# Optimization experiments

Measured on AMD Instinct MI355X. Metric: run time of the kernel, lower is better.

Reference implementation:

```python
import jax, jax.numpy as jnp
import numpy as np

N_HEAD = 8  # config.n_head

def _ln(x, g, b):
    # eqx.nn.LayerNorm, eps=1e-5
    m = x.mean(-1, keepdims=True)
    v = ((x - m) ** 2).mean(-1, keepdims=True)
    return (x - m) / jnp.sqrt(v + 1e-5) * g + b

def _lin(x, w, b):
    # eqx.nn.Linear: weight [out, in]
    return x @ w.T + b

def _heads(t):
    B, T, C = t.shape
    return t.reshape(B, T, N_HEAD, C // N_HEAD).transpose(0, 2, 1, 3)  # [B,H,T,d]

def _merge(t):
    B, H, T, d = t.shape
    return t.transpose(0, 2, 1, 3).reshape(B, T, H * d)

def setup_inputs() -> dict:
    key = jax.random.key(0)
    B, T1, T2, C, INNER, NIN = 4, 4096, 4096, 512, 2048, 2
    ks = jax.random.split(key, 16)
    w = lambda k, *s: 0.02 * jax.random.normal(k, s, dtype=jnp.float32)
    return {
        'x': jax.random.normal(ks[0], (B, T1, C), dtype=jnp.float32),
        'ys': jax.random.normal(ks[1], (NIN, B, T2, C), dtype=jnp.float32),
        'ln1_g': jnp.ones((C,)), 'ln1_b': jnp.zeros((C,)),
        'ln2_g': jnp.ones((NIN, C)), 'ln2_b': jnp.zeros((NIN, C)),
        'ln3_g': jnp.ones((C,)), 'ln3_b': jnp.zeros((C,)),
        'ln4_g': jnp.ones((C,)), 'ln4_b': jnp.zeros((C,)),
        'ln5_g': jnp.ones((C,)), 'ln5_b': jnp.zeros((C,)),
        'ca_wq': w(ks[2], C, C), 'ca_bq': jnp.zeros((C,)),
        'ca_wk': w(ks[3], NIN, C, C), 'ca_bk': jnp.zeros((NIN, C)),
        'ca_wv': w(ks[4], NIN, C, C), 'ca_bv': jnp.zeros((NIN, C)),
        'ca_wo': w(ks[5], C, C), 'ca_bo': jnp.zeros((C,)),
        'sa_wq': w(ks[6], C, C), 'sa_bq': jnp.zeros((C,)),
        'sa_wk': w(ks[7], C, C), 'sa_bk': jnp.zeros((C,)),
        'sa_wv': w(ks[8], C, C), 'sa_bv': jnp.zeros((C,)),
        'sa_wo': w(ks[9], C, C), 'sa_bo': jnp.zeros((C,)),
        'ffn1_w1': w(ks[10], INNER, C), 'ffn1_b1': jnp.zeros((INNER,)),
        'ffn1_w2': w(ks[11], C, INNER), 'ffn1_b2': jnp.zeros((C,)),
        'ffn2_w1': w(ks[12], INNER, C), 'ffn2_b1': jnp.zeros((INNER,)),
        'ffn2_w2': w(ks[13], C, INNER), 'ffn2_b2': jnp.zeros((C,)),
    }

def reference(x, ys, ln1_g, ln1_b, ln2_g, ln2_b, ln3_g, ln3_b, ln4_g, ln4_b, ln5_g, ln5_b,
              ca_wq, ca_bq, ca_wk, ca_bk, ca_wv, ca_bv, ca_wo, ca_bo,
              sa_wq, sa_bq, sa_wk, sa_bk, sa_wv, sa_bv, sa_wo, sa_bo,
              ffn1_w1, ffn1_b1, ffn1_w2, ffn1_b2, ffn2_w1, ffn2_b1, ffn2_w2, ffn2_b2):
    n_inputs = ys.shape[0]
    # ---- linear cross attention ----
    xn = _ln(x, ln1_g, ln1_b)
    q = jax.nn.softmax(_heads(_lin(xn, ca_wq, ca_bq)), axis=-1)  # [B,H,T1,d]
    out = q
    for i in range(n_inputs):  # small fixed branch count
        yn = _ln(ys[i], ln2_g[i], ln2_b[i])
        k = jax.nn.softmax(_heads(_lin(yn, ca_wk[i], ca_bk[i])), axis=-1)  # [B,H,T2,d]
        v = _heads(_lin(yn, ca_wv[i], ca_bv[i]))
        k_sum = k.sum(axis=-2, keepdims=True)                       # [B,H,1,d]
        D_inv = 1.0 / ((q * k_sum).sum(axis=-1, keepdims=True) + 1e-8)
        ctx = jnp.einsum('bhnd,bhnv->bhdv', k, v)                   # [B,H,d,d]
        out = out + jnp.einsum('bhqd,bhdv->bhqv', q, ctx) * D_inv
    x = x + _lin(_merge(out), ca_wo, ca_bo)
    # ---- FFN 1 ----
    xn = _ln(x, ln3_g, ln3_b)
    x = x + _lin(jax.nn.gelu(_lin(xn, ffn1_w1, ffn1_b1)), ffn1_w2, ffn1_b2)
    # ---- linear self attention (attn_type='l1') ----
    xn = _ln(x, ln4_g, ln4_b)
    q = jax.nn.softmax(_heads(_lin(xn, sa_wq, sa_bq)), axis=-1)
    k = jax.nn.softmax(_heads(_lin(xn, sa_wk, sa_bk)), axis=-1)
    v = _heads(_lin(xn, sa_wv, sa_bv))
    k_sum = k.sum(axis=-2, keepdims=True)
    D_inv = 1.0 / (q * k_sum).sum(axis=-1, keepdims=True)  # no eps in 'l1' branch
    ctx = jnp.einsum('bhnd,bhnv->bhdv', k, v)
    sa = jnp.einsum('bhqd,bhdv->bhqv', q, ctx) * D_inv + q
    x = x + _lin(_merge(sa), sa_wo, sa_bo)
    # ---- FFN 2 ----
    xn = _ln(x, ln5_g, ln5_b)
    x = x + _lin(jax.nn.gelu(_lin(xn, ffn2_w1, ffn2_b1)), ffn2_w2, ffn2_b2)
    return x
```

## Files before the change

kernel.cpp:

```cpp
#include <hip/hip_runtime.h>
#include <hip/hip_bf16.h>
#include <math.h>
#include <stdint.h>

typedef unsigned short u16;
typedef __attribute__((ext_vector_type(8))) short bh8;
typedef __attribute__((ext_vector_type(4))) float fx4;

#define DEV static __device__ __forceinline__

DEV float bf2f(u16 u){ union{unsigned u; float f;} v; v.u = ((unsigned)u)<<16; return v.f; }
DEV u16 f2bf(float f){ union{float f; unsigned u;} v; v.f = f;
  return (u16)((v.u + 0x7fffu + ((v.u>>16)&1u))>>16); }

DEV void async16(const u16* g, u16* l){
  __builtin_amdgcn_global_load_lds((__attribute__((address_space(1))) void*)(uintptr_t)g,
                                   (__attribute__((address_space(3))) void*)l, 16, 0, 0);
}

DEV float gelu_fast(float x){
  float u = 0.7978845608f*(x + 0.044715f*x*x*x);
  float e = __expf(-2.f*fabsf(u));
  float t = __fdividef(1.f - e, 1.f + e);
  t = copysignf(t, u);
  return 0.5f*x*(1.f + t);
}

struct WDesc { const float* src[14]; int off[14]; };
__global__ __launch_bounds__(256) void convw_kernel(WDesc d, u16* __restrict__ dst){
  int i = blockIdx.x*256 + threadIdx.x;
  int s = 0;
  #pragma unroll
  for(int j=1;j<14;j++) if(i >= d.off[j]) s = j;
  dst[i] = f2bf(d.src[s][i - d.off[s]]);
}

DEV float wsum64(float s){
  s += __shfl_xor(s,1,64);  s += __shfl_xor(s,2,64);  s += __shfl_xor(s,4,64);
  s += __shfl_xor(s,8,64);  s += __shfl_xor(s,16,64); s += __shfl_xor(s,32,64);
  return s;
}
DEV void ln_row(const float* xrow, const float* g, const float* bta, u16* orow, int lane){
  const float4* xr = (const float4*)xrow + lane*2;
  float4 a = xr[0], c = xr[1];
  float s = a.x+a.y+a.z+a.w + c.x+c.y+c.z+c.w;
  float mean = wsum64(s) * (1.f/512.f);
  float d0=a.x-mean,d1=a.y-mean,d2=a.z-mean,d3=a.w-mean;
  float d4=c.x-mean,d5=c.y-mean,d6=c.z-mean,d7=c.w-mean;
  float sv = d0*d0+d1*d1+d2*d2+d3*d3+d4*d4+d5*d5+d6*d6+d7*d7;
  float rstd = rsqrtf(wsum64(sv)*(1.f/512.f) + 1e-5f);
  const float4* gr = (const float4*)g   + lane*2;
  const float4* br = (const float4*)bta + lane*2;
  float4 g0=gr[0], g1=gr[1], b0=br[0], b1=br[1];
  bh8 o;
  o[0]=(short)f2bf(d0*rstd*g0.x+b0.x); o[1]=(short)f2bf(d1*rstd*g0.y+b0.y);
  o[2]=(short)f2bf(d2*rstd*g0.z+b0.z); o[3]=(short)f2bf(d3*rstd*g0.w+b0.w);
  o[4]=(short)f2bf(d4*rstd*g1.x+b1.x); o[5]=(short)f2bf(d5*rstd*g1.y+b1.y);
  o[6]=(short)f2bf(d6*rstd*g1.z+b1.z); o[7]=(short)f2bf(d7*rstd*g1.w+b1.w);
  *(bh8*)(orow + lane*8) = o;
}
__global__ __launch_bounds__(256) void ln_kernel(const float* __restrict__ x,
    const float* __restrict__ g, const float* __restrict__ bta, u16* __restrict__ out){
  int row  = blockIdx.x*4 + (threadIdx.x>>6);
  ln_row(x + (size_t)row*512, g, bta, out + (size_t)row*512, threadIdx.x&63);
}
__global__ __launch_bounds__(256) void lny_kernel(const float* __restrict__ ys,
    const float* __restrict__ g2, const float* __restrict__ b2, u16* __restrict__ out){
  int row  = blockIdx.x*4 + (threadIdx.x>>6);
  int i = row>>14;
  ln_row(ys + (size_t)row*512, g2 + i*512, b2 + i*512, out + (size_t)row*512, threadIdx.x&63);
}

#define GEMM_KLOOP(Ab, Wb, K)                                                        \
  const int srow = w*32 + (lane>>2);                                                 \
  const int scol = (((lane&3) ^ ((srow>>1)&3)) * 8);                                 \
  const int rsw  = ((l15>>1)&3) ^ quad;                                              \
  for(int k0=0;k0<K;k0+=32){                                                         \
    __syncthreads();                                                                 \
    async16(Ab + (size_t)srow*K      + k0 + scol, &lsA[(w*32   )*32]);               \
    async16(Ab + (size_t)(srow+16)*K + k0 + scol, &lsA[(w*32+16)*32]);               \
    async16(Wb + (size_t)srow*K      + k0 + scol, &lsB[(w*32   )*32]);               \
    async16(Wb + (size_t)(srow+16)*K + k0 + scol, &lsB[(w*32+16)*32]);               \
    __syncthreads();                                                                 \
    bh8 af[4], bfx[4];                                                               \
    _Pragma("unroll")                                                                \
    for(int t=0;t<4;t++){                                                            \
      af[t]  = *(const bh8*)&lsA[(wm*64+t*16+l15)*32 + rsw*8];                       \
      bfx[t] = *(const bh8*)&lsB[(wn*64+t*16+l15)*32 + rsw*8];                       \
    }                                                                                \
    _Pragma("unroll")                                                                \
    for(int mt=0;mt<4;mt++)                                                          \
      _Pragma("unroll")                                                              \
      for(int nt=0;nt<4;nt++)                                                        \
        acc[mt][nt] = __builtin_amdgcn_mfma_f32_16x16x32_bf16(af[mt], bfx[nt], acc[mt][nt], 0,0,0); \
  }

struct SubD { const float* bias; u16* out; float* ksum; int mode; };
struct Subs3 { SubD s[3]; };
__global__ __launch_bounds__(256) void gemm_qkv(const u16* __restrict__ A,
    const u16* __restrict__ W, Subs3 subs, int K, int wstride, int bstride, int ksstride){
  __shared__ __align__(16) u16 lsA[128*32];
  __shared__ __align__(16) u16 lsB[128*32];
  const int tid = threadIdx.x, lane = tid&63, w = tid>>6;
  const int quad = lane>>4, l15 = lane&15;
  const int bn = blockIdx.x, bm = blockIdx.y;
  const int iset = bm>>7;
  const int wm = w&1, wn = w>>1;
  fx4 acc[4][4];
  #pragma unroll
  for(int i=0;i<4;i++)
    #pragma unroll
    for(int j=0;j<4;j++) acc[i][j] = (fx4){0.f,0.f,0.f,0.f};
  const u16* Ab = A + (size_t)bm*128*K;
  const u16* Wb = W + (size_t)iset*wstride + (size_t)bn*128*K;
  GEMM_KLOOP(Ab, Wb, K)
  const SubD sub = subs.s[bn>>2];
  const int colw = (bn&3)*128 + wn*64;
  const float* bias = sub.bias + iset*bstride;
  float bcol[4];
  #pragma unroll
  for(int nt=0;nt<4;nt++) bcol[nt] = bias[colw + nt*16 + l15];

  if(sub.mode==1){
    float ksacc[4] = {0.f,0.f,0.f,0.f};
    #pragma unroll
    for(int mt=0;mt<4;mt++)
      #pragma unroll
      for(int r=0;r<4;r++){
        float v0=acc[mt][0][r]+bcol[0], v1=acc[mt][1][r]+bcol[1];
        float v2=acc[mt][2][r]+bcol[2], v3=acc[mt][3][r]+bcol[3];
        float mx = fmaxf(fmaxf(v0,v1),fmaxf(v2,v3));
        mx = fmaxf(mx,__shfl_xor(mx,1,64)); mx = fmaxf(mx,__shfl_xor(mx,2,64));
        mx = fmaxf(mx,__shfl_xor(mx,4,64)); mx = fmaxf(mx,__shfl_xor(mx,8,64));
        float e0=__expf(v0-mx), e1=__expf(v1-mx), e2=__expf(v2-mx), e3=__expf(v3-mx);
        float s = e0+e1+e2+e3;
        s += __shfl_xor(s,1,64); s += __shfl_xor(s,2,64);
        s += __shfl_xor(s,4,64); s += __shfl_xor(s,8,64);
        float inv = __fdividef(1.f, s);
        e0*=inv; e1*=inv; e2*=inv; e3*=inv;
        ksacc[0]+=e0; ksacc[1]+=e1; ksacc[2]+=e2; ksacc[3]+=e3;
        int row = bm*128 + wm*64 + mt*16 + quad*4 + r;
        size_t rb = (size_t)row*512;
        sub.out[rb+colw+ 0+l15]=f2bf(e0); sub.out[rb+colw+16+l15]=f2bf(e1);
        sub.out[rb+colw+32+l15]=f2bf(e2); sub.out[rb+colw+48+l15]=f2bf(e3);
      }
    if(sub.ksum){
      int b = (bm&127)>>5;
      float* ks = sub.ksum + iset*ksstride + b*512;
      #pragma unroll
      for(int nt=0;nt<4;nt++){
        float s = ksacc[nt];
        s += __shfl_xor(s,16,64); s += __shfl_xor(s,32,64);
        if(quad==0) atomicAdd(&ks[colw + nt*16 + l15], s);
      }
    }
  } else {
    #pragma unroll
    for(int mt=0;mt<4;mt++)
      #pragma unroll
      for(int r=0;r<4;r++){
        int row = bm*128 + wm*64 + mt*16 + quad*4 + r;
        size_t rb = (size_t)row*512;
        #pragma unroll
        for(int nt=0;nt<4;nt++)
          sub.out[rb + colw + nt*16 + l15] = f2bf(acc[mt][nt][r] + bcol[nt]);
      }
  }
}

template<int EPI>
__global__ __launch_bounds__(256) void gemm_bt(const u16* __restrict__ A,
    const u16* __restrict__ W, const float* __restrict__ bias,
    const float* __restrict__ res, void* __restrict__ out, int N, int K){
  __shared__ __align__(16) u16 lsA[128*32];
  __shared__ __align__(16) u16 lsB[128*32];
  const int tid = threadIdx.x, lane = tid&63, w = tid>>6;
  const int quad = lane>>4, l15 = lane&15;
  const int bn = blockIdx.x, bm = blockIdx.y;
  const int wm = w&1, wn = w>>1;
  fx4 acc[4][4];
  #pragma unroll
  for(int i=0;i<4;i++)
    #pragma unroll
    for(int j=0;j<4;j++) acc[i][j] = (fx4){0.f,0.f,0.f,0.f};
  const u16* Ab = A + (size_t)bm*128*K;
  const u16* Wb = W + (size_t)bn*128*K;
  GEMM_KLOOP(Ab, Wb, K)
  const int colbase = bn*128 + wn*64;
  float bcol[4];
  #pragma unroll
  for(int nt=0;nt<4;nt++) bcol[nt] = bias[colbase + nt*16 + l15];

  if(EPI==3){
    float* of = (float*)out;
    #pragma unroll
    for(int mt=0;mt<4;mt++)
      #pragma unroll
      for(int r=0;r<4;r++){
        int row = bm*128 + wm*64 + mt*16 + quad*4 + r;
        size_t rb = (size_t)row*N;
        #pragma unroll
        for(int nt=0;nt<4;nt++){
          int col = colbase + nt*16 + l15;
          of[rb+col] = res[rb+col] + acc[mt][nt][r] + bcol[nt];
        }
      }
  } else {
    u16* ob = (u16*)out;
    #pragma unroll
    for(int mt=0;mt<4;mt++)
      #pragma unroll
      for(int r=0;r<4;r++){
        int row = bm*128 + wm*64 + mt*16 + quad*4 + r;
        size_t rb = (size_t)row*N;
        #pragma unroll
        for(int nt=0;nt<4;nt++)
          ob[rb + colbase + nt*16 + l15] = f2bf(gelu_fast(acc[mt][nt][r] + bcol[nt]));
      }
  }
}

__global__ __launch_bounds__(256) void ctx_kernel(const u16* __restrict__ kb,
    const u16* __restrict__ vb, float* __restrict__ ctx, size_t kstride){
  __shared__ __align__(16) u16 lk[64*72];
  __shared__ __align__(16) u16 lv[64*72];
  const int tid=threadIdx.x, lane=tid&63, w=tid>>6, quad=lane>>4, l15=lane&15;
  const int bh2 = blockIdx.x, i = bh2>>5, h = bh2&7, b = (bh2>>3)&3;
  const u16* kbase = kb + (size_t)i*kstride;
  const u16* vbase = vb + (size_t)i*kstride;
  const size_t rowbase = (size_t)b*4096 + (size_t)blockIdx.y*512;
  const int mt0=(w&1)*32, nt0=(w>>1)*32;
  fx4 acc[2][2];
  #pragma unroll
  for(int x=0;x<2;x++)
    #pragma unroll
    for(int j=0;j<2;j++) acc[x][j] = (fx4){0.f,0.f,0.f,0.f};
  const int tl = tid>>2, part = tid&3;
  for(int it=0; it<8; it++){
    __syncthreads();
    {
      size_t gro = (rowbase + it*64 + tl)*512 + h*64 + part*16;
      bh8 k0 = *(const bh8*)(kbase + gro); bh8 k1 = *(const bh8*)(kbase + gro + 8);
      bh8 v0 = *(const bh8*)(vbase + gro); bh8 v1 = *(const bh8*)(vbase + gro + 8);
      #pragma unroll
      for(int j=0;j<8;j++){
        lk[(part*16+j  )*72 + tl] = (u16)k0[j];
        lk[(part*16+8+j)*72 + tl] = (u16)k1[j];
        lv[(part*16+j  )*72 + tl] = (u16)v0[j];
        lv[(part*16+8+j)*72 + tl] = (u16)v1[j];
      }
    }
    __syncthreads();
    #pragma unroll
    for(int ks=0;ks<2;ks++){
      bh8 a0 = *(const bh8*)&lk[(mt0    +l15)*72 + ks*32 + quad*8];
      bh8 a1 = *(const bh8*)&lk[(mt0+16 +l15)*72 + ks*32 + quad*8];
      bh8 b0 = *(const bh8*)&lv[(nt0    +l15)*72 + ks*32 + quad*8];
      bh8 b1 = *(const bh8*)&lv[(nt0+16 +l15)*72 + ks*32 + quad*8];
      acc[0][0] = __builtin_amdgcn_mfma_f32_16x16x32_bf16(a0,b0,acc[0][0],0,0,0);
      acc[0][1] = __builtin_amdgcn_mfma_f32_16x16x32_bf16(a0,b1,acc[0][1],0,0,0);
      acc[1][0] = __builtin_amdgcn_mfma_f32_16x16x32_bf16(a1,b0,acc[1][0],0,0,0);
      acc[1][1] = __builtin_amdgcn_mfma_f32_16x16x32_bf16(a1,b1,acc[1][1],0,0,0);
    }
  }
  float* cb = ctx + (size_t)bh2*4096;
  #pragma unroll
  for(int mi=0;mi<2;mi++)
    #pragma unroll
    for(int ni=0;ni<2;ni++)
      #pragma unroll
      for(int r=0;r<4;r++){
        int d1 = mt0 + mi*16 + quad*4 + r;
        int d2 = nt0 + ni*16 + l15;
        atomicAdd(&cb[d1*64 + d2], acc[mi][ni][r]);
      }
}

template<int NIN>
__global__ __launch_bounds__(256) void apply_kernel(const u16* __restrict__ q,
    const float* __restrict__ ctx, const float* __restrict__ ksum, float eps,
    u16* __restrict__ out){
  __shared__ __align__(16) u16 lctx[(NIN+1)*64*72];
  const int tid=threadIdx.x, lane=tid&63, w=tid>>6, quad=lane>>4, l15=lane&15;
  const int bh = blockIdx.x, b=bh>>3, h=bh&7;
  {
    int base = tid*16;
    int d1 = base>>6, d2b = base&63;
    #pragma unroll
    for(int s=0;s<=NIN;s++){
      u16* dst = &lctx[s*64*72];
      if(s<NIN){
        const float* sp = ctx + ((size_t)s*32 + bh)*4096 + base;
        #pragma unroll
        for(int j=0;j<16;j++) dst[(d2b+j)*72 + d1] = f2bf(sp[j]);
      } else {
        #pragma unroll
        for(int j=0;j<16;j++) dst[(d2b+j)*72 + d1] = ((d2b+j)==d1) ? (u16)0x3f80 : (u16)0;
      }
    }
  }
  float kslo[NIN][8], kshi[NIN][8];
  #pragma unroll
  for(int s=0;s<NIN;s++){
    const float* ks = ksum + s*2048 + b*512 + h*64;
    #pragma unroll
    for(int j=0;j<8;j++){ kslo[s][j] = ks[quad*8+j]; kshi[s][j] = ks[32+quad*8+j]; }
  }
  __syncthreads();
  bh8 bfr[NIN+1][4][2];
  #pragma unroll
  for(int s=0;s<=NIN;s++)
    #pragma unroll
    for(int nt=0;nt<4;nt++)
      #pragma unroll
      for(int ks=0;ks<2;ks++)
        bfr[s][nt][ks] = *(const bh8*)&lctx[s*64*72 + (nt*16+l15)*72 + ks*32 + quad*8];
  const size_t tb0 = (size_t)b*4096 + (size_t)blockIdx.y*256 + w*64;
  for(int g=0;g<4;g++){
    size_t tb = tb0 + g*16;
    const u16* qr = q + (tb + l15)*512 + h*64;
    bh8 a0 = *(const bh8*)(qr + quad*8);
    bh8 a1 = *(const bh8*)(qr + 32 + quad*8);
    float dv[NIN][4];
    #pragma unroll
    for(int s=0;s<NIN;s++){
      float part = 0.f;
      #pragma unroll
      for(int j=0;j<8;j++)
        part += bf2f((u16)a0[j])*kslo[s][j] + bf2f((u16)a1[j])*kshi[s][j];
      part += __shfl_xor(part,16,64); part += __shfl_xor(part,32,64);
      #pragma unroll
      for(int r=0;r<4;r++)
        dv[s][r] = __fdividef(1.f, __shfl(part, quad*4+r, 64) + eps);
    }
    fx4 outv[4];
    #pragma unroll
    for(int nt=0;nt<4;nt++) outv[nt] = (fx4){0.f,0.f,0.f,0.f};
    #pragma unroll
    for(int s=0;s<=NIN;s++){
      fx4 c[4];
      #pragma unroll
      for(int nt=0;nt<4;nt++){
        c[nt] = (fx4){0.f,0.f,0.f,0.f};
        c[nt] = __builtin_amdgcn_mfma_f32_16x16x32_bf16(a0, bfr[s][nt][0], c[nt], 0,0,0);
        c[nt] = __builtin_amdgcn_mfma_f32_16x16x32_bf16(a1, bfr[s][nt][1], c[nt], 0,0,0);
      }
      #pragma unroll
      for(int nt=0;nt<4;nt++)
        #pragma unroll
        for(int r=0;r<4;r++) outv[nt][r] += c[nt][r]*((s==NIN)?1.f:dv[s][r]);
    }
    #pragma unroll
    for(int nt=0;nt<4;nt++)
      #pragma unroll
      for(int r=0;r<4;r++)
        out[(tb+quad*4+r)*512 + h*64 + nt*16 + l15] = f2bf(outv[nt][r]);
  }
}

extern "C" void kernel_launch(void* const* d_in, const int* in_sizes, int n_in,
                              void* d_out, int out_size, void* d_ws, size_t ws_size,
                              hipStream_t stream){
  const float* x_in =(const float*)d_in[0];
  const float* ys   =(const float*)d_in[1];
  const float* ln1g =(const float*)d_in[2],  *ln1b=(const float*)d_in[3];
  const float* ln2g =(const float*)d_in[4],  *ln2b=(const float*)d_in[5];
  const float* ln3g =(const float*)d_in[6],  *ln3b=(const float*)d_in[7];
  const float* ln4g =(const float*)d_in[8],  *ln4b=(const float*)d_in[9];
  const float* ln5g =(const float*)d_in[10], *ln5b=(const float*)d_in[11];
  const float* ca_wq=(const float*)d_in[12], *ca_bq=(const float*)d_in[13];
  const float* ca_wk=(const float*)d_in[14], *ca_bk=(const float*)d_in[15];
  const float* ca_wv=(const float*)d_in[16], *ca_bv=(const float*)d_in[17];
  const float* ca_wo=(const float*)d_in[18], *ca_bo=(const float*)d_in[19];
  const float* sa_wq=(const float*)d_in[20], *sa_bq=(const float*)d_in[21];
  const float* sa_wk=(const float*)d_in[22], *sa_bk=(const float*)d_in[23];
  const float* sa_wv=(const float*)d_in[24], *sa_bv=(const float*)d_in[25];
  const float* sa_wo=(const float*)d_in[26], *sa_bo=(const float*)d_in[27];
  const float* f1w1 =(const float*)d_in[28], *f1b1=(const float*)d_in[29];
  const float* f1w2 =(const float*)d_in[30], *f1b2=(const float*)d_in[31];
  const float* f2w1 =(const float*)d_in[32], *f2b1=(const float*)d_in[33];
  const float* f2w2 =(const float*)d_in[34], *f2b2=(const float*)d_in[35];

  char* p = (char*)d_ws;
  u16*   WBF = (u16*)p;    p += 13631488;
  float* XW  = (float*)p;  p += 33554432;
  u16*   XN2 = (u16*)p;    p += 33554432;
  u16*   QB  = (u16*)p;    p += 16777216;
  u16*   R1  = (u16*)p;    p += 67108864;
  u16*   OUTB= (u16*)p;    p += 16777216;
  float* SM  = (float*)p;  p += 1597440;
  u16*   XN  = XN2;
  u16*   KB2 = R1;
  u16*   VB2 = R1 + 16777216;
  u16*   HB  = R1;
  float* CTXC = SM;
  float* CTXS = SM + 262144;
  float* KSC  = SM + 393216;
  float* KSS  = SM + 397312;

  WDesc wd;
  const float* wsrc[14] = {ca_wq, ca_wk, ca_wv, ca_wk+262144, ca_wv+262144, ca_wo,
                           sa_wq, sa_wk, sa_wv, sa_wo, f1w1, f1w2, f2w1, f2w2};
  const int    woff[14] = {0, 262144, 524288, 786432, 1048576, 1310720,
                           1572864, 1835008, 2097152, 2359296,
                           2621440, 3670016, 4718592, 5767168};
  for(int i=0;i<14;i++){ wd.src[i]=wsrc[i]; wd.off[i]=woff[i]; }
  convw_kernel<<<26624,256,0,stream>>>(wd, WBF);
  hipMemsetAsync(SM, 0, 399360*sizeof(float), stream);

  SubD zsub = {nullptr,nullptr,nullptr,0};

  ln_kernel<<<4096,256,0,stream>>>(x_in, ln1g, ln1b, XN);
  { Subs3 s = {{ {ca_bq, QB, nullptr, 1}, zsub, zsub }};
    gemm_qkv<<<dim3(4,128),256,0,stream>>>(XN, WBF+0, s, 512, 0,0,0); }
  lny_kernel<<<8192,256,0,stream>>>(ys, ln2g, ln2b, XN2);
  { Subs3 s = {{ {ca_bk, KB2, KSC, 1}, {ca_bv, VB2, nullptr, 0}, zsub }};
    gemm_qkv<<<dim3(8,256),256,0,stream>>>(XN2, WBF+262144, s, 512,
                                           524288, 512, 2048); }
  ctx_kernel<<<dim3(64,8),256,0,stream>>>(KB2, VB2, CTXC, (size_t)16384*512);
  apply_kernel<2><<<dim3(32,16),256,0,stream>>>(QB, CTXC, KSC, 1e-8f, OUTB);
  gemm_bt<3><<<dim3(4,128),256,0,stream>>>(OUTB, WBF+1310720, ca_bo, x_in, XW, 512, 512);

  ln_kernel<<<4096,256,0,stream>>>(XW, ln3g, ln3b, XN);
  gemm_bt<2><<<dim3(16,128),256,0,stream>>>(XN, WBF+2621440, f1b1, nullptr, HB, 2048, 512);
  gemm_bt<3><<<dim3(4,128),256,0,stream>>>(HB, WBF+3670016, f1b2, XW, XW, 512, 2048);

  ln_kernel<<<4096,256,0,stream>>>(XW, ln4g, ln4b, XN);
  { Subs3 s = {{ {sa_bq, QB, nullptr, 1}, {sa_bk, KB2, KSS, 1}, {sa_bv, VB2, nullptr, 0} }};
    gemm_qkv<<<dim3(12,128),256,0,stream>>>(XN, WBF+1572864, s, 512, 0,0,0); }
  ctx_kernel<<<dim3(32,8),256,0,stream>>>(KB2, VB2, CTXS, 0);
  apply_kernel<1><<<dim3(32,16),256,0,stream>>>(QB, CTXS, KSS, 0.f, OUTB);
  gemm_bt<3><<<dim3(4,128),256,0,stream>>>(OUTB, WBF+2359296, sa_bo, XW, XW, 512, 512);

  ln_kernel<<<4096,256,0,stream>>>(XW, ln5g, ln5b, XN);
  gemm_bt<2><<<dim3(16,128),256,0,stream>>>(XN, WBF+4718592, f2b1, nullptr, HB, 2048, 512);
  gemm_bt<3><<<dim3(4,128),256,0,stream>>>(HB, WBF+5767168, f2b2, XW, (float*)d_out, 512, 2048);
}
```

Baseline: 770.1 us.

## Double-buffer GEMM LDS tiles and swizzle workgroups across XCDs

The GEMM k-loop now uses two LDS buffers, so the async global-to-LDS loads for the next k-slice are issued before the MFMAs on the current one, and one of the two barriers per iteration is dropped. Both GEMM kernels also remap the block index so consecutive tiles land on the same XCD, which should improve L2 reuse of A and W tiles. The cost is doubled LDS per block (32KB), which may lower occupancy. The swizzle assumes the workgroup count is divisible by 8.

```diff
diff --git a/kernel.cpp b/kernel.cpp
--- a/kernel.cpp
+++ b/kernel.cpp
@@ -24,6 +24,14 @@
   float t = __fdividef(1.f - e, 1.f + e);
   t = copysignf(t, u);
   return 0.5f*x*(1.f + t);
+}
+
+DEV int2 xcd_swz(){
+  const int gx  = gridDim.x;
+  const int ord = blockIdx.y*gx + blockIdx.x;
+  const int nwg = gx*gridDim.y;
+  const int wg  = (ord&7)*(nwg>>3) + (ord>>3);
+  int2 r; r.x = wg % gx; r.y = wg / gx; return r;
 }
 
 struct WDesc { const float* src[14]; int off[14]; };
@@ -71,39 +79,45 @@
   ln_row(ys + (size_t)row*512, g2 + i*512, b2 + i*512, out + (size_t)row*512, threadIdx.x&63);
 }
 
+#define GEMM_STAGE(Ab, Wb, K, kk, buf)                                               \
+    async16(Ab + (size_t)srow*(K)      + (kk) + scol, &lsA[buf][(w*32   )*32]);      \
+    async16(Ab + (size_t)(srow+16)*(K) + (kk) + scol, &lsA[buf][(w*32+16)*32]);      \
+    async16(Wb + (size_t)srow*(K)      + (kk) + scol, &lsB[buf][(w*32   )*32]);      \
+    async16(Wb + (size_t)(srow+16)*(K) + (kk) + scol, &lsB[buf][(w*32+16)*32]);
+
 #define GEMM_KLOOP(Ab, Wb, K)                                                        \
   const int srow = w*32 + (lane>>2);                                                 \
   const int scol = (((lane&3) ^ ((srow>>1)&3)) * 8);                                 \
   const int rsw  = ((l15>>1)&3) ^ quad;                                              \
+  { GEMM_STAGE(Ab, Wb, K, 0, 0) }                                                    \
+  __syncthreads();                                                                   \
   for(int k0=0;k0<K;k0+=32){                                                         \
-    __syncthreads();                                                                 \
-    async16(Ab + (size_t)srow*K      + k0 + scol, &lsA[(w*32   )*32]);               \
-    async16(Ab + (size_t)(srow+16)*K + k0 + scol, &lsA[(w*32+16)*32]);               \
-    async16(Wb + (size_t)srow*K      + k0 + scol, &lsB[(w*32   )*32]);               \
-    async16(Wb + (size_t)(srow+16)*K + k0 + scol, &lsB[(w*32+16)*32]);               \
-    __syncthreads();                                                                 \
+    const int cur = (k0>>5)&1;                                                       \
+    if(k0+32 < K){ GEMM_STAGE(Ab, Wb, K, k0+32, cur^1) }                             \
     bh8 af[4], bfx[4];                                                               \
     _Pragma("unroll")                                                                \
     for(int t=0;t<4;t++){                                                            \
-      af[t]  = *(const bh8*)&lsA[(wm*64+t*16+l15)*32 + rsw*8];                       \
-      bfx[t] = *(const bh8*)&lsB[(wn*64+t*16+l15)*32 + rsw*8];                       \
+      af[t]  = *(const bh8*)&lsA[cur][(wm*64+t*16+l15)*32 + rsw*8];                  \
+      bfx[t] = *(const bh8*)&lsB[cur][(wn*64+t*16+l15)*32 + rsw*8];                  \
     }                                                                                \
     _Pragma("unroll")                                                                \
     for(int mt=0;mt<4;mt++)                                                          \
       _Pragma("unroll")                                                              \
       for(int nt=0;nt<4;nt++)                                                        \
         acc[mt][nt] = __builtin_amdgcn_mfma_f32_16x16x32_bf16(af[mt], bfx[nt], acc[mt][nt], 0,0,0); \
+    __syncthreads();                                                                 \
   }
 
 struct SubD { const float* bias; u16* out; float* ksum; int mode; };
 struct Subs3 { SubD s[3]; };
 __global__ __launch_bounds__(256) void gemm_qkv(const u16* __restrict__ A,
     const u16* __restrict__ W, Subs3 subs, int K, int wstride, int bstride, int ksstride){
-  __shared__ __align__(16) u16 lsA[128*32];
-  __shared__ __align__(16) u16 lsB[128*32];
+  __shared__ __align__(16) u16 lsA[2][128*32];
+  __shared__ __align__(16) u16 lsB[2][128*32];
   const int tid = threadIdx.x, lane = tid&63, w = tid>>6;
   const int quad = lane>>4, l15 = lane&15;
-  const int bn = blockIdx.x, bm = blockIdx.y;
+  const int2 swz = xcd_swz();
+  const int bn = swz.x, bm = swz.y;
   const int iset = bm>>7;
   const int wm = w&1, wn = w>>1;
   fx4 acc[4][4];
@@ -172,11 +186,12 @@
 __global__ __launch_bounds__(256) void gemm_bt(const u16* __restrict__ A,
     const u16* __restrict__ W, const float* __restrict__ bias,
     const float* __restrict__ res, void* __restrict__ out, int N, int K){
-  __shared__ __align__(16) u16 lsA[128*32];
-  __shared__ __align__(16) u16 lsB[128*32];
+  __shared__ __align__(16) u16 lsA[2][128*32];
+  __shared__ __align__(16) u16 lsB[2][128*32];
   const int tid = threadIdx.x, lane = tid&63, w = tid>>6;
   const int quad = lane>>4, l15 = lane&15;
-  const int bn = blockIdx.x, bm = blockIdx.y;
+  const int2 swz = xcd_swz();
+  const int bn = swz.x, bm = swz.y;
   const int wm = w&1, wn = w>>1;
   fx4 acc[4][4];
   #pragma unroll
```

Result: faster. 705.5 us (-8.4%).
